# Performance work log

Measured on AMD Instinct MI355X. Metric: run time of the kernel, lower is better.

The kernel has to match this reference:

```python
import jax, jax.numpy as jnp
import numpy as np

B, S, D, H = 2, 2048, 1024, 16
DK = D // H  # 64


def setup_inputs() -> dict:
    key = jax.random.key(0)
    k0, k1, k2, k3, k4, k5, k6 = jax.random.split(key, 7)
    scale = 0.02
    return {
        "q": jax.random.normal(k0, (B, S, D), dtype=jnp.float32),
        "k": jax.random.normal(k1, (B, S, D), dtype=jnp.float32),
        "v": jax.random.normal(k2, (B, S, D), dtype=jnp.float32),
        # per-head Q/K projection weights (n_head separate Linear layers, bias=False)
        "Wq": jax.random.normal(k3, (H, D, DK), dtype=jnp.float32) * scale,
        "Wk": jax.random.normal(k4, (H, D, DK), dtype=jnp.float32) * scale,
        # shared V projection (the same v_layer object is reused for every head)
        "Wv": jax.random.normal(k5, (D, DK), dtype=jnp.float32) * scale,
        # output projection fc: d_v -> d_model, bias=False
        "Wo": jax.random.normal(k6, (DK, D), dtype=jnp.float32) * scale,
    }


def reference(q, k, v, Wq, Wk, Wv, Wo):
    d_k = Wq.shape[-1]
    # batched per-head projections (replaces the Python loop over heads)
    qs = jnp.einsum("bsd,hdk->bhsk", q, Wq)          # [B,H,S,DK]
    ks = jnp.einsum("bsd,hdk->bhsk", k, Wk)          # [B,H,S,DK]
    vs = jnp.einsum("bsd,dk->bsk", v, Wv)            # [B,S,DK] shared across heads
    scores = jnp.einsum("bhsk,bhtk->bhst", qs, ks) / jnp.sqrt(
        jnp.asarray(d_k, dtype=jnp.float32)
    )                                                 # [B,H,S,S]
    attn = jax.nn.softmax(scores, axis=-1)            # [B,H,S,S]; dropout = identity (eval)
    heads = jnp.einsum("bhst,btk->bhsk", attn, vs)    # [B,H,S,DK]
    head = heads.mean(axis=1)                         # mean over heads, not concat
    attn_mean = attn.mean(axis=1)                     # [B,S,S]
    out = jnp.einsum("bsk,kd->bsd", head, Wo)         # [B,S,D]; dropout = identity
    return (out, attn_mean)
```

## Files before the change

kernel.cpp:

```cpp
#include <hip/hip_runtime.h>

#define B_ 2
#define S_ 2048
#define D_ 1024
#define H_ 16
#define DK_ 64

typedef __bf16 bf8 __attribute__((ext_vector_type(8)));
typedef float f4 __attribute__((ext_vector_type(4)));
typedef unsigned short u16x8 __attribute__((ext_vector_type(8)));

__device__ __forceinline__ unsigned short f2bf_bits(float f) {
  unsigned int u = __float_as_uint(f);
  return (unsigned short)((u + 0x7fffu + ((u >> 16) & 1u)) >> 16);
}

__device__ __forceinline__ bf8 pack_bf8(f4 lo, f4 hi) {
  u16x8 u;
  u[0] = f2bf_bits(lo[0]); u[1] = f2bf_bits(lo[1]);
  u[2] = f2bf_bits(lo[2]); u[3] = f2bf_bits(lo[3]);
  u[4] = f2bf_bits(hi[0]); u[5] = f2bf_bits(hi[1]);
  u[6] = f2bf_bits(hi[2]); u[7] = f2bf_bits(hi[3]);
  union { u16x8 u; bf8 b; } x; x.u = u; return x.b;
}

__device__ __forceinline__ bf8 ldb(const unsigned short* p) {
  return *reinterpret_cast<const bf8*>(p);
}

__device__ __forceinline__ void stage16(const void* g, void* l) {
  __builtin_amdgcn_global_load_lds(
      (const __attribute__((address_space(1))) void*)g,
      (__attribute__((address_space(3))) void*)l, 16, 0, 0);
}

#define MFMA(a, b, c) __builtin_amdgcn_mfma_f32_16x16x32_bf16((a), (b), (c), 0, 0, 0)

__global__ void k_prep(const float* __restrict__ q, const float* __restrict__ k,
                       const float* __restrict__ wq, const float* __restrict__ wk,
                       const float* __restrict__ wv, const float* __restrict__ wo,
                       unsigned short* __restrict__ qb, unsigned short* __restrict__ kb,
                       unsigned short* __restrict__ wqt, unsigned short* __restrict__ wkt,
                       unsigned short* __restrict__ wvt, unsigned short* __restrict__ wot) {
  __shared__ float tl[64 * 65];
  int bid = blockIdx.x, tid = threadIdx.x;
  const int rr = tid >> 6, cc = tid & 63;
  if (bid < 4096) {
    int which = bid >> 11;
    long i = ((long)(bid & 2047) * 256 + tid) * 8;
    const float* src = which ? k : q;
    unsigned short* dst = which ? kb : qb;
    f4 lo = *reinterpret_cast<const f4*>(src + i);
    f4 hi = *reinterpret_cast<const f4*>(src + i + 4);
    *reinterpret_cast<bf8*>(dst + i) = pack_bf8(lo, hi);
  } else if (bid < 4352) {
    int blk = bid - 4096;
    int h = blk >> 4, d0 = (blk & 15) * 64;
    for (int m = 0; m < 2; ++m) {
      const float* src = m ? wk : wq;
      unsigned short* dst = m ? wkt : wqt;
      if (m) __syncthreads();
#pragma unroll
      for (int it = 0; it < 16; ++it) {
        int d = it * 4 + rr;
        tl[cc * 65 + d] = src[(long)h * 65536 + (d0 + d) * 64 + cc];
      }
      __syncthreads();
#pragma unroll
      for (int it = 0; it < 16; ++it) {
        int n = it * 4 + rr;
        dst[(long)h * 65536 + n * 1024 + d0 + cc] = f2bf_bits(tl[n * 65 + cc]);
      }
    }
  } else if (bid < 4368) {
    int d0 = (bid - 4352) * 64;
#pragma unroll
    for (int it = 0; it < 16; ++it) {
      int d = it * 4 + rr;
      tl[cc * 65 + d] = wv[(long)(d0 + d) * 64 + cc];
    }
    __syncthreads();
#pragma unroll
    for (int it = 0; it < 16; ++it) {
      int n = it * 4 + rr;
      wvt[(long)n * 1024 + d0 + cc] = f2bf_bits(tl[n * 65 + cc]);
    }
  } else {
    int d0 = (bid - 4368) * 64;
#pragma unroll
    for (int it = 0; it < 16; ++it) {
      int kk = it * 4 + rr;
      tl[cc * 65 + kk] = wo[(long)kk * 1024 + d0 + cc];
    }
    __syncthreads();
#pragma unroll
    for (int it = 0; it < 16; ++it) {
      int ddl = it * 4 + rr;
      wot[(long)(d0 + ddl) * 64 + cc] = f2bf_bits(tl[ddl * 65 + cc]);
    }
  }
}

__global__ __launch_bounds__(256) void k_gemm_qk(
    const unsigned short* __restrict__ qb, const unsigned short* __restrict__ kb,
    const unsigned short* __restrict__ wqt, const unsigned short* __restrict__ wkt,
    unsigned short* __restrict__ qsb, unsigned short* __restrict__ ksb) {
  __shared__ unsigned short lds[8192];
  const int tid = threadIdx.x, wave = tid >> 6, lane = tid & 63;
  const int l15 = lane & 15, quad = lane >> 4;
  const int m0 = blockIdx.x * 128, n0 = blockIdx.y * 128;
  const int which = blockIdx.z;
  const unsigned short* A = which ? kb : qb;
  const unsigned short* W = which ? wkt : wqt;
  unsigned short* C = which ? ksb : qsb;
  const float scale = which ? 1.0f : 0.18033688011112042f;
  const int wr = wave >> 1, wc = wave & 1;

  f4 acc[4][4];
#pragma unroll
  for (int i = 0; i < 4; ++i)
#pragma unroll
    for (int j = 0; j < 4; ++j) acc[i][j] = f4{0.f, 0.f, 0.f, 0.f};

  const int sl15 = tid & 15, squad = (tid >> 4) & 3, st = tid >> 6;
  const unsigned short* gA = A + (long)(m0 + st * 16 + sl15) * D_ + squad * 8;
  const unsigned short* gB = W + (long)(n0 + st * 16 + sl15) * D_ + squad * 8;

  for (int k0 = 0; k0 < D_; k0 += 32) {
    stage16(gA + k0, lds + tid * 8);
    stage16(gA + 64 * D_ + k0, lds + 2048 + tid * 8);
    stage16(gB + k0, lds + 4096 + tid * 8);
    stage16(gB + 64 * D_ + k0, lds + 6144 + tid * 8);
    __syncthreads();
    bf8 aF[4], bF[4];
#pragma unroll
    for (int mi = 0; mi < 4; ++mi)
      aF[mi] = ldb(lds + (wr * 4 + mi) * 512 + lane * 8);
#pragma unroll
    for (int ni = 0; ni < 4; ++ni)
      bF[ni] = ldb(lds + 4096 + (wc * 4 + ni) * 512 + lane * 8);
#pragma unroll
    for (int mi = 0; mi < 4; ++mi)
#pragma unroll
      for (int ni = 0; ni < 4; ++ni)
        acc[mi][ni] = MFMA(aF[mi], bF[ni], acc[mi][ni]);
    __syncthreads();
  }
#pragma unroll
  for (int mi = 0; mi < 4; ++mi)
#pragma unroll
    for (int r = 0; r < 4; ++r) {
      long row = m0 + wr * 64 + mi * 16 + quad * 4 + r;
#pragma unroll
      for (int ni = 0; ni < 4; ++ni)
        C[row * D_ + n0 + wc * 64 + ni * 16 + l15] = f2bf_bits(acc[mi][ni][r] * scale);
    }
}

__global__ __launch_bounds__(256) void k_pv(
    const float* __restrict__ v, const unsigned short* __restrict__ wvt,
    float* __restrict__ pv) {
  const int tid = threadIdx.x, wave = tid >> 6, lane = tid & 63;
  const int l15 = lane & 15, quad = lane >> 4;
  const int rg = blockIdx.x, kc = blockIdx.y;
  const int row0 = rg * 64 + wave * 16;
  const float* arow = v + (long)(row0 + l15) * D_ + kc * 256 + quad * 8;
  const unsigned short* wbase = wvt + kc * 256 + quad * 8;
  f4 acc[4];
  for (int i = 0; i < 4; ++i) acc[i] = f4{0.f, 0.f, 0.f, 0.f};
  for (int k0 = 0; k0 < 256; k0 += 32) {
    f4 alo = *reinterpret_cast<const f4*>(arow + k0);
    f4 ahi = *reinterpret_cast<const f4*>(arow + k0 + 4);
    bf8 a = pack_bf8(alo, ahi);
#pragma unroll
    for (int i = 0; i < 4; ++i) {
      bf8 bf = ldb(wbase + (long)(i * 16 + l15) * D_ + k0);
      acc[i] = MFMA(a, bf, acc[i]);
    }
  }
#pragma unroll
  for (int i = 0; i < 4; ++i)
#pragma unroll
    for (int r = 0; r < 4; ++r)
      pv[((long)kc * 4096 + row0 + quad * 4 + r) * 64 + i * 16 + l15] = acc[i][r];
}

__global__ void k_vred(const float* __restrict__ pv, unsigned short* __restrict__ vst) {
  int e = blockIdx.x * 256 + threadIdx.x;
  int t = e & 2047, dk = (e >> 11) & 63, b = e >> 17;
  long row = (long)b * S_ + t;
  float s = pv[row * 64 + dk] + pv[(4096 + row) * 64 + dk] +
            pv[(8192 + row) * 64 + dk] + pv[(12288 + row) * 64 + dk];
  vst[e] = f2bf_bits(s);
}

__global__ __launch_bounds__(512) void k_denom(
    const unsigned short* __restrict__ qsb, const unsigned short* __restrict__ ksb,
    float* __restrict__ recip) {
  __shared__ unsigned short lds[8192];
  const int tid = threadIdx.x, wave = tid >> 6, lane = tid & 63;
  const int l15 = lane & 15, quad = lane >> 4;
  const int stile = blockIdx.x, h = blockIdx.y, b = blockIdx.z;
  const int s0 = stile * 128 + wave * 16;

  const unsigned short* qrow = qsb + ((long)(b * S_) + s0 + l15) * D_ + h * 64 + quad * 8;
  bf8 a0 = ldb(qrow);
  bf8 a1 = ldb(qrow + 32);

  f4 sum = f4{0.f, 0.f, 0.f, 0.f};
  for (int t0 = 0; t0 < S_; t0 += 128) {
#pragma unroll
    for (int i = 0; i < 2; ++i) {
      int u = i * 512 + tid;
      int sl15 = u & 15, squad = (u >> 4) & 3, stt = (u >> 6) & 7, sh2 = u >> 9;
      stage16(ksb + ((long)(b * S_) + t0 + stt * 16 + sl15) * D_ + h * 64 + sh2 * 32 + squad * 8,
              lds + u * 8);
    }
    __syncthreads();
#pragma unroll
    for (int tt = 0; tt < 8; ++tt) {
      bf8 b0 = ldb(lds + tt * 512 + lane * 8);
      bf8 b1 = ldb(lds + 4096 + tt * 512 + lane * 8);
      f4 d = f4{0.f, 0.f, 0.f, 0.f};
      d = MFMA(a0, b0, d);
      d = MFMA(a1, b1, d);
#pragma unroll
      for (int r = 0; r < 4; ++r) sum[r] += __builtin_amdgcn_exp2f(d[r]);
    }
    __syncthreads();
  }
#pragma unroll
  for (int m = 1; m < 16; m <<= 1) {
#pragma unroll
    for (int r = 0; r < 4; ++r) sum[r] += __shfl_xor(sum[r], m, 64);
  }
  if (l15 == 0) {
    float* rp = recip + (long)(b * H_ + h) * S_ + s0 + quad * 4;
#pragma unroll
    for (int r = 0; r < 4; ++r) rp[r] = 1.0f / (16.0f * sum[r]);
  }
}

__global__ __launch_bounds__(512) void k_attn(
    const unsigned short* __restrict__ qsb, const unsigned short* __restrict__ ksb,
    const float* __restrict__ recip, float* __restrict__ am) {
  __shared__ unsigned short lds[8192];
  const int tid = threadIdx.x, wave = tid >> 6, lane = tid & 63;
  const int l15 = lane & 15, quad = lane >> 4;
  const int tchunk = blockIdx.x, stile = blockIdx.y, b = blockIdx.z;
  const int s0 = stile * 128 + wave * 16;
  const int t0c = tchunk * 128;

  f4 acc[8];
#pragma unroll
  for (int tt = 0; tt < 8; ++tt) acc[tt] = f4{0.f, 0.f, 0.f, 0.f};

  const unsigned short* qbase = qsb + ((long)(b * S_) + s0 + l15) * D_ + quad * 8;

  for (int h = 0; h < H_; ++h) {
#pragma unroll
    for (int i = 0; i < 2; ++i) {
      int u = i * 512 + tid;
      int sl15 = u & 15, squad = (u >> 4) & 3, stt = (u >> 6) & 7, sh2 = u >> 9;
      stage16(ksb + ((long)(b * S_) + t0c + stt * 16 + sl15) * D_ + h * 64 + sh2 * 32 + squad * 8,
              lds + u * 8);
    }
    bf8 a0 = ldb(qbase + h * 64);
    bf8 a1 = ldb(qbase + h * 64 + 32);
    f4 rp = *reinterpret_cast<const f4*>(recip + (long)(b * H_ + h) * S_ + s0 + quad * 4);
    __syncthreads();
#pragma unroll
    for (int tt = 0; tt < 8; ++tt) {
      bf8 b0 = ldb(lds + tt * 512 + lane * 8);
      bf8 b1 = ldb(lds + 4096 + tt * 512 + lane * 8);
      f4 d = f4{0.f, 0.f, 0.f, 0.f};
      d = MFMA(a0, b0, d);
      d = MFMA(a1, b1, d);
#pragma unroll
      for (int r = 0; r < 4; ++r) acc[tt][r] += rp[r] * __builtin_amdgcn_exp2f(d[r]);
    }
    __syncthreads();
  }
  float* obase = am + ((long)b * S_ + s0 + quad * 4) * S_ + t0c + l15;
#pragma unroll
  for (int tt = 0; tt < 8; ++tt)
#pragma unroll
    for (int r = 0; r < 4; ++r) obase[(long)r * S_ + tt * 16] = acc[tt][r];
}

__global__ __launch_bounds__(256) void k_hpart(
    const float* __restrict__ am, const unsigned short* __restrict__ vst,
    float* __restrict__ ph) {
  const int tid = threadIdx.x, wave = tid >> 6, lane = tid & 63;
  const int l15 = lane & 15, quad = lane >> 4;
  const int rg = blockIdx.x, kc = blockIdx.y;
  const int row0 = rg * 64 + wave * 16;
  const int b = row0 >> 11;
  const float* arow = am + (long)(row0 + l15) * S_ + kc * 512 + quad * 8;
  const unsigned short* vb = vst + (long)b * DK_ * S_ + kc * 512 + quad * 8;
  f4 acc[4];
  for (int i = 0; i < 4; ++i) acc[i] = f4{0.f, 0.f, 0.f, 0.f};
  for (int t0 = 0; t0 < 512; t0 += 32) {
    f4 alo = *reinterpret_cast<const f4*>(arow + t0);
    f4 ahi = *reinterpret_cast<const f4*>(arow + t0 + 4);
    bf8 a = pack_bf8(alo, ahi);
#pragma unroll
    for (int i = 0; i < 4; ++i) {
      bf8 bf = ldb(vb + (long)(i * 16 + l15) * S_ + t0);
      acc[i] = MFMA(a, bf, acc[i]);
    }
  }
#pragma unroll
  for (int i = 0; i < 4; ++i)
#pragma unroll
    for (int r = 0; r < 4; ++r)
      ph[((long)kc * 4096 + row0 + quad * 4 + r) * 64 + i * 16 + l15] = acc[i][r];
}

__global__ void k_hred(const float* __restrict__ ph, unsigned short* __restrict__ headb) {
  int e = blockIdx.x * 256 + threadIdx.x;
  float s = ph[e] + ph[e + 4096 * 64] + ph[e + 2 * 4096 * 64] + ph[e + 3 * 4096 * 64];
  headb[e] = f2bf_bits(s);
}

__global__ __launch_bounds__(256) void k_out(
    const unsigned short* __restrict__ head, const unsigned short* __restrict__ wot,
    float* __restrict__ out) {
  const int tid = threadIdx.x, wave = tid >> 6, lane = tid & 63;
  const int l15 = lane & 15, quad = lane >> 4;
  const int dchunk = blockIdx.x, stile = blockIdx.y, b = blockIdx.z;
  const int s0 = stile * 64 + wave * 16;
  const int n0 = dchunk * 128;
  const unsigned short* hrow = head + ((long)b * S_ + s0 + l15) * DK_ + quad * 8;
  bf8 a0 = ldb(hrow);
  bf8 a1 = ldb(hrow + 32);
  const unsigned short* wb = wot + quad * 8;
  float* obase = out + ((long)b * S_ + s0 + quad * 4) * D_ + n0 + l15;
#pragma unroll
  for (int i = 0; i < 8; ++i) {
    const unsigned short* wp = wb + (long)(n0 + i * 16 + l15) * DK_;
    bf8 b0 = ldb(wp);
    bf8 b1 = ldb(wp + 32);
    f4 d = f4{0.f, 0.f, 0.f, 0.f};
    d = MFMA(a0, b0, d);
    d = MFMA(a1, b1, d);
#pragma unroll
    for (int r = 0; r < 4; ++r) obase[(long)r * D_ + i * 16] = d[r];
  }
}

extern "C" void kernel_launch(void* const* d_in, const int* in_sizes, int n_in,
                              void* d_out, int out_size, void* d_ws, size_t ws_size,
                              hipStream_t stream) {
  const float* q  = (const float*)d_in[0];
  const float* k  = (const float*)d_in[1];
  const float* v  = (const float*)d_in[2];
  const float* Wq = (const float*)d_in[3];
  const float* Wk = (const float*)d_in[4];
  const float* Wv = (const float*)d_in[5];
  const float* Wo = (const float*)d_in[6];

  float* out = (float*)d_out;
  float* am  = out + (long)B_ * S_ * D_;

  unsigned short* qsb  = (unsigned short*)d_ws;
  unsigned short* ksb  = qsb + 4194304;
  unsigned short* wqt  = ksb + 4194304;
  unsigned short* wkt  = wqt + 1048576;
  unsigned short* wvt  = wkt + 1048576;
  unsigned short* wot  = wvt + 65536;
  unsigned short* vst  = wot + 65536;
  unsigned short* headb= vst + 262144;
  float* recip = (float*)(headb + 262144);

  unsigned short* qb = (unsigned short*)am;
  unsigned short* kb = qb + 4194304;
  float* part = out;

  k_prep<<<4384, 256, 0, stream>>>(q, k, Wq, Wk, Wv, Wo, qb, kb, wqt, wkt, wvt, wot);
  k_gemm_qk<<<dim3(32, 8, 2), 256, 0, stream>>>(qb, kb, wqt, wkt, qsb, ksb);
  k_pv<<<dim3(64, 4), 256, 0, stream>>>(v, wvt, part);
  k_vred<<<1024, 256, 0, stream>>>(part, vst);
  k_denom<<<dim3(16, 16, 2), 512, 0, stream>>>(qsb, ksb, recip);
  k_attn<<<dim3(16, 16, 2), 512, 0, stream>>>(qsb, ksb, recip, am);
  k_hpart<<<dim3(64, 4), 256, 0, stream>>>(am, vst, part);
  k_hred<<<1024, 256, 0, stream>>>(part, headb);
  k_out<<<dim3(8, 32, 2), 256, 0, stream>>>(headb, wot, out);
}
```

Before: 247.4 us.

## Split denominator and attention-map kernels over key halves, process two heads per stage

```diff
diff --git a/kernel.cpp b/kernel.cpp
--- a/kernel.cpp
+++ b/kernel.cpp
@@ -194,13 +194,14 @@
   vst[e] = f2bf_bits(s);
 }
 
-__global__ __launch_bounds__(512) void k_denom(
+__global__ __launch_bounds__(512, 8) void k_denom(
     const unsigned short* __restrict__ qsb, const unsigned short* __restrict__ ksb,
-    float* __restrict__ recip) {
+    float* __restrict__ dpart) {
   __shared__ unsigned short lds[8192];
   const int tid = threadIdx.x, wave = tid >> 6, lane = tid & 63;
   const int l15 = lane & 15, quad = lane >> 4;
-  const int stile = blockIdx.x, h = blockIdx.y, b = blockIdx.z;
+  const int stile = blockIdx.x >> 1, tc = blockIdx.x & 1;
+  const int h = blockIdx.y, b = blockIdx.z;
   const int s0 = stile * 128 + wave * 16;
 
   const unsigned short* qrow = qsb + ((long)(b * S_) + s0 + l15) * D_ + h * 64 + quad * 8;
@@ -208,7 +209,7 @@
   bf8 a1 = ldb(qrow + 32);
 
   f4 sum = f4{0.f, 0.f, 0.f, 0.f};
-  for (int t0 = 0; t0 < S_; t0 += 128) {
+  for (int t0 = tc * 1024; t0 < tc * 1024 + 1024; t0 += 128) {
 #pragma unroll
     for (int i = 0; i < 2; ++i) {
       int u = i * 512 + tid;
@@ -235,55 +236,75 @@
     for (int r = 0; r < 4; ++r) sum[r] += __shfl_xor(sum[r], m, 64);
   }
   if (l15 == 0) {
-    float* rp = recip + (long)(b * H_ + h) * S_ + s0 + quad * 4;
-#pragma unroll
-    for (int r = 0; r < 4; ++r) rp[r] = 1.0f / (16.0f * sum[r]);
-  }
-}
-
-__global__ __launch_bounds__(512) void k_attn(
+    float* rp = dpart + (long)tc * 65536 + (long)(b * H_ + h) * S_ + s0 + quad * 4;
+#pragma unroll
+    for (int r = 0; r < 4; ++r) rp[r] = sum[r];
+  }
+}
+
+__global__ __launch_bounds__(512, 8) void k_attn(
     const unsigned short* __restrict__ qsb, const unsigned short* __restrict__ ksb,
-    const float* __restrict__ recip, float* __restrict__ am) {
+    const float* __restrict__ dpart, float* __restrict__ am) {
   __shared__ unsigned short lds[8192];
   const int tid = threadIdx.x, wave = tid >> 6, lane = tid & 63;
   const int l15 = lane & 15, quad = lane >> 4;
   const int tchunk = blockIdx.x, stile = blockIdx.y, b = blockIdx.z;
   const int s0 = stile * 128 + wave * 16;
-  const int t0c = tchunk * 128;
-
-  f4 acc[8];
-#pragma unroll
-  for (int tt = 0; tt < 8; ++tt) acc[tt] = f4{0.f, 0.f, 0.f, 0.f};
+  const int t0c = tchunk * 64;
+
+  f4 acc[4];
+#pragma unroll
+  for (int tt = 0; tt < 4; ++tt) acc[tt] = f4{0.f, 0.f, 0.f, 0.f};
 
   const unsigned short* qbase = qsb + ((long)(b * S_) + s0 + l15) * D_ + quad * 8;
-
-  for (int h = 0; h < H_; ++h) {
-#pragma unroll
-    for (int i = 0; i < 2; ++i) {
-      int u = i * 512 + tid;
-      int sl15 = u & 15, squad = (u >> 4) & 3, stt = (u >> 6) & 7, sh2 = u >> 9;
-      stage16(ksb + ((long)(b * S_) + t0c + stt * 16 + sl15) * D_ + h * 64 + sh2 * 32 + squad * 8,
-              lds + u * 8);
-    }
+  const int sl15 = tid & 15, squad = (tid >> 4) & 3, stt = (tid >> 6) & 3, sh2 = (tid >> 8) & 1;
+  const unsigned short* kst =
+      ksb + ((long)(b * S_) + t0c + stt * 16 + sl15) * D_ + sh2 * 32 + squad * 8;
+  const float* pbase = dpart + (long)(b * H_) * S_ + s0 + quad * 4;
+
+  for (int h = 0; h < H_; h += 2) {
+    stage16(kst + h * 64, lds + tid * 8);
+    stage16(kst + (h + 1) * 64, lds + 4096 + tid * 8);
     bf8 a0 = ldb(qbase + h * 64);
     bf8 a1 = ldb(qbase + h * 64 + 32);
-    f4 rp = *reinterpret_cast<const f4*>(recip + (long)(b * H_ + h) * S_ + s0 + quad * 4);
-    __syncthreads();
-#pragma unroll
-    for (int tt = 0; tt < 8; ++tt) {
+    bf8 a2 = ldb(qbase + (h + 1) * 64);
+    bf8 a3 = ldb(qbase + (h + 1) * 64 + 32);
+    f4 p0a = *reinterpret_cast<const f4*>(pbase + (long)h * S_);
+    f4 p0b = *reinterpret_cast<const f4*>(pbase + (long)h * S_ + 65536);
+    f4 p1a = *reinterpret_cast<const f4*>(pbase + (long)(h + 1) * S_);
+    f4 p1b = *reinterpret_cast<const f4*>(pbase + (long)(h + 1) * S_ + 65536);
+    f4 rp0, rp1;
+#pragma unroll
+    for (int r = 0; r < 4; ++r) {
+      rp0[r] = __builtin_amdgcn_rcpf(16.0f * (p0a[r] + p0b[r]));
+      rp1[r] = __builtin_amdgcn_rcpf(16.0f * (p1a[r] + p1b[r]));
+    }
+    __syncthreads();
+#pragma unroll
+    for (int tt = 0; tt < 4; ++tt) {
       bf8 b0 = ldb(lds + tt * 512 + lane * 8);
-      bf8 b1 = ldb(lds + 4096 + tt * 512 + lane * 8);
+      bf8 b1 = ldb(lds + 2048 + tt * 512 + lane * 8);
       f4 d = f4{0.f, 0.f, 0.f, 0.f};
       d = MFMA(a0, b0, d);
       d = MFMA(a1, b1, d);
 #pragma unroll
-      for (int r = 0; r < 4; ++r) acc[tt][r] += rp[r] * __builtin_amdgcn_exp2f(d[r]);
+      for (int r = 0; r < 4; ++r) acc[tt][r] += rp0[r] * __builtin_amdgcn_exp2f(d[r]);
+    }
+#pragma unroll
+    for (int tt = 0; tt < 4; ++tt) {
+      bf8 c0 = ldb(lds + 4096 + tt * 512 + lane * 8);
+      bf8 c1 = ldb(lds + 6144 + tt * 512 + lane * 8);
+      f4 e = f4{0.f, 0.f, 0.f, 0.f};
+      e = MFMA(a2, c0, e);
+      e = MFMA(a3, c1, e);
+#pragma unroll
+      for (int r = 0; r < 4; ++r) acc[tt][r] += rp1[r] * __builtin_amdgcn_exp2f(e[r]);
     }
     __syncthreads();
   }
   float* obase = am + ((long)b * S_ + s0 + quad * 4) * S_ + t0c + l15;
 #pragma unroll
-  for (int tt = 0; tt < 8; ++tt)
+  for (int tt = 0; tt < 4; ++tt)
 #pragma unroll
     for (int r = 0; r < 4; ++r) obase[(long)r * S_ + tt * 16] = acc[tt][r];
 }
@@ -371,18 +392,18 @@
   unsigned short* wot  = wvt + 65536;
   unsigned short* vst  = wot + 65536;
   unsigned short* headb= vst + 262144;
-  float* recip = (float*)(headb + 262144);
 
   unsigned short* qb = (unsigned short*)am;
   unsigned short* kb = qb + 4194304;
   float* part = out;
+  float* dpart = out + 2097152;
 
   k_prep<<<4384, 256, 0, stream>>>(q, k, Wq, Wk, Wv, Wo, qb, kb, wqt, wkt, wvt, wot);
   k_gemm_qk<<<dim3(32, 8, 2), 256, 0, stream>>>(qb, kb, wqt, wkt, qsb, ksb);
   k_pv<<<dim3(64, 4), 256, 0, stream>>>(v, wvt, part);
   k_vred<<<1024, 256, 0, stream>>>(part, vst);
-  k_denom<<<dim3(16, 16, 2), 512, 0, stream>>>(qsb, ksb, recip);
-  k_attn<<<dim3(16, 16, 2), 512, 0, stream>>>(qsb, ksb, recip, am);
+  k_denom<<<dim3(32, 16, 2), 512, 0, stream>>>(qsb, ksb, dpart);
+  k_attn<<<dim3(32, 16, 2), 512, 0, stream>>>(qsb, ksb, dpart, am);
   k_hpart<<<dim3(64, 4), 256, 0, stream>>>(am, vst, part);
   k_hred<<<1024, 256, 0, stream>>>(part, headb);
   k_out<<<dim3(8, 32, 2), 256, 0, stream>>>(headb, wot, out);
```

New measurement: 284.5 us. 15.0% more time.

## Double-buffer K tiles in LDS for denominator and attention-mean kernels

Applied to the files above, without the earlier changes.

```diff
diff --git a/kernel.cpp b/kernel.cpp
--- a/kernel.cpp
+++ b/kernel.cpp
@@ -197,7 +197,7 @@
 __global__ __launch_bounds__(512) void k_denom(
     const unsigned short* __restrict__ qsb, const unsigned short* __restrict__ ksb,
     float* __restrict__ recip) {
-  __shared__ unsigned short lds[8192];
+  __shared__ unsigned short lds[16384];
   const int tid = threadIdx.x, wave = tid >> 6, lane = tid & 63;
   const int l15 = lane & 15, quad = lane >> 4;
   const int stile = blockIdx.x, h = blockIdx.y, b = blockIdx.z;
@@ -207,27 +207,42 @@
   bf8 a0 = ldb(qrow);
   bf8 a1 = ldb(qrow + 32);
 
+  const int sl15 = tid & 15, squad = (tid >> 4) & 3, stt = (tid >> 6) & 7;
+  const unsigned short* g0 =
+      ksb + ((long)(b * S_) + stt * 16 + sl15) * D_ + h * 64 + squad * 8;
+
+  stage16(g0, lds + tid * 8);
+  stage16(g0 + 32, lds + 4096 + tid * 8);
+  asm volatile("s_waitcnt vmcnt(0)" ::: "memory");
+  __builtin_amdgcn_s_barrier();
+  int cur = 0;
+
   f4 sum = f4{0.f, 0.f, 0.f, 0.f};
-  for (int t0 = 0; t0 < S_; t0 += 128) {
-#pragma unroll
-    for (int i = 0; i < 2; ++i) {
-      int u = i * 512 + tid;
-      int sl15 = u & 15, squad = (u >> 4) & 3, stt = (u >> 6) & 7, sh2 = u >> 9;
-      stage16(ksb + ((long)(b * S_) + t0 + stt * 16 + sl15) * D_ + h * 64 + sh2 * 32 + squad * 8,
-              lds + u * 8);
-    }
-    __syncthreads();
+  for (int it = 0; it < 16; ++it) {
+    if (it + 1 < 16) {
+      const unsigned short* gn = g0 + (long)(it + 1) * 128 * D_;
+      unsigned short* nb = lds + (cur ^ 1) * 8192;
+      stage16(gn, nb + tid * 8);
+      stage16(gn + 32, nb + 4096 + tid * 8);
+    }
+    const unsigned short* base = lds + cur * 8192;
+    __builtin_amdgcn_s_setprio(1);
 #pragma unroll
     for (int tt = 0; tt < 8; ++tt) {
-      bf8 b0 = ldb(lds + tt * 512 + lane * 8);
-      bf8 b1 = ldb(lds + 4096 + tt * 512 + lane * 8);
+      bf8 b0 = ldb(base + tt * 512 + lane * 8);
+      bf8 b1 = ldb(base + 4096 + tt * 512 + lane * 8);
       f4 d = f4{0.f, 0.f, 0.f, 0.f};
       d = MFMA(a0, b0, d);
       d = MFMA(a1, b1, d);
 #pragma unroll
       for (int r = 0; r < 4; ++r) sum[r] += __builtin_amdgcn_exp2f(d[r]);
     }
-    __syncthreads();
+    __builtin_amdgcn_s_setprio(0);
+    if (it + 1 < 16) {
+      asm volatile("s_waitcnt vmcnt(0)" ::: "memory");
+      __builtin_amdgcn_s_barrier();
+      cur ^= 1;
+    }
   }
 #pragma unroll
   for (int m = 1; m < 16; m <<= 1) {
@@ -244,7 +259,7 @@
 __global__ __launch_bounds__(512) void k_attn(
     const unsigned short* __restrict__ qsb, const unsigned short* __restrict__ ksb,
     const float* __restrict__ recip, float* __restrict__ am) {
-  __shared__ unsigned short lds[8192];
+  __shared__ unsigned short lds[16384];
   const int tid = threadIdx.x, wave = tid >> 6, lane = tid & 63;
   const int l15 = lane & 15, quad = lane >> 4;
   const int tchunk = blockIdx.x, stile = blockIdx.y, b = blockIdx.z;
@@ -256,30 +271,45 @@
   for (int tt = 0; tt < 8; ++tt) acc[tt] = f4{0.f, 0.f, 0.f, 0.f};
 
   const unsigned short* qbase = qsb + ((long)(b * S_) + s0 + l15) * D_ + quad * 8;
+  const int sl15 = tid & 15, squad = (tid >> 4) & 3, stt = (tid >> 6) & 7;
+  const unsigned short* g0 =
+      ksb + ((long)(b * S_) + t0c + stt * 16 + sl15) * D_ + squad * 8;
+  const float* rbase = recip + (long)(b * H_) * S_ + s0 + quad * 4;
+
+  stage16(g0, lds + tid * 8);
+  stage16(g0 + 32, lds + 4096 + tid * 8);
+  asm volatile("s_waitcnt vmcnt(0)" ::: "memory");
+  __builtin_amdgcn_s_barrier();
+  int cur = 0;
 
   for (int h = 0; h < H_; ++h) {
-#pragma unroll
-    for (int i = 0; i < 2; ++i) {
-      int u = i * 512 + tid;
-      int sl15 = u & 15, squad = (u >> 4) & 3, stt = (u >> 6) & 7, sh2 = u >> 9;
-      stage16(ksb + ((long)(b * S_) + t0c + stt * 16 + sl15) * D_ + h * 64 + sh2 * 32 + squad * 8,
-              lds + u * 8);
+    if (h + 1 < H_) {
+      const unsigned short* gn = g0 + (h + 1) * 64;
+      unsigned short* nb = lds + (cur ^ 1) * 8192;
+      stage16(gn, nb + tid * 8);
+      stage16(gn + 32, nb + 4096 + tid * 8);
     }
     bf8 a0 = ldb(qbase + h * 64);
     bf8 a1 = ldb(qbase + h * 64 + 32);
-    f4 rp = *reinterpret_cast<const f4*>(recip + (long)(b * H_ + h) * S_ + s0 + quad * 4);
-    __syncthreads();
+    f4 rp = *reinterpret_cast<const f4*>(rbase + (long)h * S_);
+    const unsigned short* base = lds + cur * 8192;
+    __builtin_amdgcn_s_setprio(1);
 #pragma unroll
     for (int tt = 0; tt < 8; ++tt) {
-      bf8 b0 = ldb(lds + tt * 512 + lane * 8);
-      bf8 b1 = ldb(lds + 4096 + tt * 512 + lane * 8);
+      bf8 b0 = ldb(base + tt * 512 + lane * 8);
+      bf8 b1 = ldb(base + 4096 + tt * 512 + lane * 8);
       f4 d = f4{0.f, 0.f, 0.f, 0.f};
       d = MFMA(a0, b0, d);
       d = MFMA(a1, b1, d);
 #pragma unroll
       for (int r = 0; r < 4; ++r) acc[tt][r] += rp[r] * __builtin_amdgcn_exp2f(d[r]);
     }
-    __syncthreads();
+    __builtin_amdgcn_s_setprio(0);
+    if (h + 1 < H_) {
+      asm volatile("s_waitcnt vmcnt(0)" ::: "memory");
+      __builtin_amdgcn_s_barrier();
+      cur ^= 1;
+    }
   }
   float* obase = am + ((long)b * S_ + s0 + quad * 4) * S_ + t0c + l15;
 #pragma unroll
```

After: 243.5 us. About the same (-1.6%).
